# Performance work log

Hardware: AMD Instinct MI355X
Metric: run time of the kernel (lower is better)

The kernel has to match this reference:

```python
import jax, jax.numpy as jnp
import numpy as np

B, C, H, W = 16, 256, 32, 32
EPS = 1e-6


def setup_inputs() -> dict:
    key = jax.random.key(0)
    ks = jax.random.split(key, 6)
    s = 1.0 / np.sqrt(C)  # conv-like init scale
    return {
        "x": jax.random.normal(ks[0], (B, C, H, W), dtype=jnp.float32),
        "ln_w": jnp.ones((C,), dtype=jnp.float32),
        "ln_b": jnp.zeros((C,), dtype=jnp.float32),
        "wq": jax.random.normal(ks[1], (C, C), dtype=jnp.float32) * s,
        "bq": jnp.zeros((C,), dtype=jnp.float32),
        "wk": jax.random.normal(ks[2], (C, C), dtype=jnp.float32) * s,
        "bk": jnp.zeros((C,), dtype=jnp.float32),
        "wv": jax.random.normal(ks[3], (C, C), dtype=jnp.float32) * s,
        "bv": jnp.zeros((C,), dtype=jnp.float32),
        "wp": jax.random.normal(ks[4], (C, C), dtype=jnp.float32) * s,
        "bp": jnp.zeros((C,), dtype=jnp.float32),
    }


def reference(x, ln_w, ln_b, wq, bq, wk, bk, wv, bv, wp, bp):
    b, c, h, w = x.shape
    n = h * w
    # LayerNorm2d: normalize over channel dim (biased variance)
    mean = jnp.mean(x, axis=1, keepdims=True)
    var = jnp.var(x, axis=1, keepdims=True)
    hn = (x - mean) / jnp.sqrt(var + EPS)
    hn = hn * ln_w[None, :, None, None] + ln_b[None, :, None, None]
    hn = hn.reshape(b, c, n)  # [B, C, N]
    # 1x1 convs == channel matmuls; tokens layout [B, N, C]
    q = jnp.einsum('oc,bcn->bno', wq, hn) + bq  # [B, N, C]
    k = jnp.einsum('oc,bcn->bon', wk, hn) + bk[None, :, None]  # [B, C, N]
    v = jnp.einsum('oc,bcn->bno', wv, hn) + bv  # [B, N, C]
    scale = c ** (-0.5)
    attn = jnp.einsum('bnc,bcm->bnm', q, k) * scale  # [B, N, N]
    attn = jax.nn.softmax(attn, axis=-1)
    # dropout is identity in eval mode (deterministic reference)
    out = jnp.einsum('bnm,bmc->bnc', attn, v)  # [B, N, C]
    out = jnp.einsum('oc,bnc->bon', wp, out) + bp[None, :, None]  # [B, C, N]
    out = out.reshape(b, c, h, w)
    return x + out
```

## Files before the change

kernel.cpp:

```cpp
#include <hip/hip_runtime.h>
#include <hip/hip_bf16.h>
#include <stdint.h>

typedef __attribute__((ext_vector_type(8))) short bf8_t;
typedef __attribute__((ext_vector_type(4))) short s4_t;
typedef __attribute__((ext_vector_type(4))) float f4_t;
typedef __attribute__((ext_vector_type(16))) float f16x_t;
typedef unsigned short u16;

#define GLOAD16(g, l) __builtin_amdgcn_global_load_lds(                                  \
    (const __attribute__((address_space(1))) void*)(g),                                  \
    (__attribute__((address_space(3))) void*)(l), 16, 0, 0)

__device__ __forceinline__ u16 f2bf(float f) {
    union { float f; unsigned u; } c; c.f = f;
    unsigned u = c.u;
    return (u16)((u + 0x7fffu + ((u >> 16) & 1u)) >> 16);
}

__device__ __forceinline__ unsigned cvt_pk_bf16(float lo, float hi_) {
    unsigned r;
    asm("v_cvt_pk_bf16_f32 %0, %1, %2" : "=v"(r) : "v"(lo), "v"(hi_));
    return r;
}

__global__ void prep_kernel(const float* __restrict__ wq, const float* __restrict__ wk,
                            const float* __restrict__ wv, const float* __restrict__ wp,
                            const float* __restrict__ bq, const float* __restrict__ bk,
                            const float* __restrict__ bv,
                            u16* __restrict__ wcat, u16* __restrict__ wpb,
                            float* __restrict__ biasc) {
    int idx = blockIdx.x * 256 + threadIdx.x;
    if (idx < 196608) {
        int o = idx >> 8, c = idx & 255;
        float v = (o < 256) ? wq[o * 256 + c]
                : (o < 512) ? wk[(o - 256) * 256 + c]
                            : wv[(o - 512) * 256 + c];
        wcat[idx] = f2bf(v);
    } else if (idx < 262144) {
        wpb[idx - 196608] = f2bf(wp[idx - 196608]);
    } else if (idx < 262912) {
        int i = idx - 262144;
        biasc[i] = (i < 256) ? bq[i] : (i < 512) ? bk[i - 256] : bv[i - 512];
    }
}

__global__ __launch_bounds__(512) void ln_kernel(const float* __restrict__ x,
                                                 const float* __restrict__ lw,
                                                 const float* __restrict__ lb,
                                                 u16* __restrict__ hn) {
    int tid = threadIdx.x;
    int tl = tid & 63, cg = tid >> 6;
    int tok = blockIdx.x * 64 + tl;
    int b = tok >> 10, n = tok & 1023;
    const float* xb = x + (size_t)b * 262144 + n;
    int ch0 = cg * 32;
    float v[32];
    float s = 0.f, s2 = 0.f;
    #pragma unroll
    for (int j = 0; j < 32; j++) {
        v[j] = xb[(size_t)(ch0 + j) * 1024];
        s += v[j]; s2 += v[j] * v[j];
    }
    __shared__ float2 red[8][64];
    red[cg][tl] = make_float2(s, s2);
    __syncthreads();
    s = 0.f; s2 = 0.f;
    #pragma unroll
    for (int g = 0; g < 8; g++) { float2 p = red[g][tl]; s += p.x; s2 += p.y; }
    float mean = s * 0.00390625f;
    float var  = s2 * 0.00390625f - mean * mean;
    float rstd = rsqrtf(var + 1e-6f);
    u16* hr = hn + (size_t)tok * 256 + ch0;
    #pragma unroll
    for (int j8 = 0; j8 < 4; j8++) {
        bf8_t pk;
        #pragma unroll
        for (int j = 0; j < 8; j++) {
            int c = j8 * 8 + j;
            float y = (v[c] - mean) * rstd * lw[ch0 + c] + lb[ch0 + c];
            pk[j] = (short)f2bf(y);
        }
        *(bf8_t*)&hr[j8 * 8] = pk;
    }
}

template <int EPI>
__global__ __launch_bounds__(256, 2) void gemm_bt(
    const u16* __restrict__ A, const u16* __restrict__ B, void* __restrict__ Cp,
    int lda, int ldb, int ldc, int nk,
    long sA, long sB, long sC,
    const float* __restrict__ aux1, const float* __restrict__ aux2,
    u16* __restrict__ ktp, u16* __restrict__ vtp) {
    __shared__ u16 lsA[128 * 32];
    __shared__ u16 lsB[128 * 32];
    const int tid = threadIdx.x;
    const int z = blockIdx.z;
    const int m0 = blockIdx.x * 128, n0 = blockIdx.y * 128;
    const int lane = tid & 63;
    const int w = tid >> 6, wm = w >> 1, wn = w & 1;
    const int lm = lane & 15, lg = lane >> 4;
    const int sr = tid >> 2, sc = (tid & 3) * 8;

    const u16* ga = A + (size_t)z * sA + (size_t)(m0 + sr) * lda + sc;
    const u16* gb = B + (size_t)z * sB + (size_t)(n0 + sr) * ldb + sc;
    u16* la  = &lsA[sr * 32 + sc];
    u16* lb2 = &lsB[sr * 32 + sc];

    f4_t acc[4][4];
    #pragma unroll
    for (int i = 0; i < 4; i++)
        #pragma unroll
        for (int j = 0; j < 4; j++) acc[i][j] = (f4_t)0.0f;

    for (int kt = 0; kt < nk; ++kt) {
        GLOAD16(ga, la);
        GLOAD16(ga + (size_t)64 * lda, la + 64 * 32);
        GLOAD16(gb, lb2);
        GLOAD16(gb + (size_t)64 * ldb, lb2 + 64 * 32);
        ga += 32; gb += 32;
        __syncthreads();
        bf8_t af[4], bfv[4];
        #pragma unroll
        for (int i = 0; i < 4; i++)
            af[i] = *(const bf8_t*)&lsA[(wm * 64 + i * 16 + lm) * 32 + lg * 8];
        #pragma unroll
        for (int i = 0; i < 4; i++)
            bfv[i] = *(const bf8_t*)&lsB[(wn * 64 + i * 16 + lm) * 32 + lg * 8];
        #pragma unroll
        for (int i = 0; i < 4; i++)
            #pragma unroll
            for (int j = 0; j < 4; j++)
                acc[i][j] = __builtin_amdgcn_mfma_f32_16x16x32_bf16(af[i], bfv[j], acc[i][j], 0, 0, 0);
        __syncthreads();
    }

    const int rb = m0 + wm * 64 + lg * 4;
    const int cb = n0 + wn * 64 + lm;
    #pragma unroll
    for (int i = 0; i < 4; i++)
        #pragma unroll
        for (int j = 0; j < 4; j++)
            #pragma unroll
            for (int r = 0; r < 4; r++) {
                int row = rb + i * 16 + r;
                int col = cb + j * 16;
                float v = acc[i][j][r];
                if (EPI == 0) {
                    float val = v + aux1[col];
                    int bb = row >> 10, n = row & 1023;
                    if (col < 256) {
                        ((u16*)Cp)[(size_t)row * 256 + col] = f2bf(val * 0.0625f);
                    } else if (col < 512) {
                        int c = col - 256;
                        ktp[(((size_t)bb * 32 + (c >> 3)) * 1024 + n) * 8 + (c & 7)] = f2bf(val);
                    } else {
                        int d = col - 512;
                        vtp[(((size_t)bb * 128 + (n >> 3)) * 256 + d) * 8 + (n & 7)] = f2bf(val);
                    }
                } else {
                    size_t idx = (size_t)z * sC + (size_t)row * ldc + col;
                    ((float*)Cp)[idx] = v + aux1[row] + aux2[idx];
                }
            }
}

__global__ __launch_bounds__(512)
__attribute__((amdgpu_waves_per_eu(2, 2)))
void flash_kernel(const u16* __restrict__ qbuf,
                  const u16* __restrict__ kt,
                  const u16* __restrict__ vt3,
                  u16* __restrict__ O) {
    __shared__ u16 K_lds[2][2][32 * 32 * 8];
    __shared__ u16 V_lds[2][2][4 * 256 * 8];
    __shared__ float mstat[2][32], lstat[2][32];

    const int flat = blockIdx.x;
    const int xcd = flat & 7, idx = flat >> 3;
    const int b = (xcd << 1) | (idx & 1);
    const int qb = idx >> 1;
    const int tid = threadIdx.x;
    const int wv = tid >> 6, lane = tid & 63;
    const int hi = lane >> 5, lq = lane & 31;
    const int qw = wv & 1, dw = (wv >> 1) & 1, g = wv >> 2;

    const int qrow = qb * 64 + qw * 32 + lq;
    const u16* qptr = qbuf + (size_t)(b * 1024 + qrow) * 256 + hi * 8;
    bf8_t qf[16];
    #pragma unroll
    for (int tc = 0; tc < 16; tc++) qf[tc] = *(const bf8_t*)(qptr + tc * 16);

    float m_r = -1e30f, l_r = 0.f;
    f16x_t o_acc[4];
    #pragma unroll
    for (int dt = 0; dt < 4; dt++) o_acc[dt] = (f16x_t)0.0f;

#define STAGE(T, BUF)                                                                     \
    {                                                                                     \
        _Pragma("unroll")                                                                 \
        for (int g2 = 0; g2 < 2; g2++) {                                                  \
            _Pragma("unroll")                                                             \
            for (int it = 0; it < 2; it++) {                                              \
                int cid = it * 512 + tid;                                                 \
                int chunk = cid >> 5, kvl = cid & 31;                                     \
                const u16* gk = kt + (((size_t)b * 32 + chunk) * 1024                     \
                                      + g2 * 512 + (T) * 32 + kvl) * 8;                   \
                GLOAD16(gk, &K_lds[g2][BUF][cid * 8]);                                    \
            }                                                                             \
            _Pragma("unroll")                                                             \
            for (int it = 0; it < 2; it++) {                                              \
                int cid = it * 512 + tid;                                                 \
                int kc = cid >> 8, d = cid & 255;                                         \
                const u16* gv = vt3 + (((size_t)b * 128 + g2 * 64 + (T) * 4 + kc) * 256   \
                                       + d) * 8;                                          \
                GLOAD16(gv, &V_lds[g2][BUF][cid * 8]);                                    \
            }                                                                             \
        }                                                                                 \
    }

    STAGE(0, 0);
    STAGE(1, 1);
    asm volatile("s_waitcnt vmcnt(8)" ::: "memory");
    __builtin_amdgcn_s_barrier();

    for (int t = 0; t < 16; ++t) {
        const int buf = t & 1;

        const u16* kb = &K_lds[g][buf][0];
        bf8_t kf[16];
        #pragma unroll
        for (int tc = 0; tc < 16; tc++)
            kf[tc] = *(const bf8_t*)(kb + ((tc * 2 + hi) * 32 + lq) * 8);

        f16x_t s0 = (f16x_t)0.0f, s1 = (f16x_t)0.0f;
        __builtin_amdgcn_s_setprio(1);
        #pragma unroll
        for (int tc = 0; tc < 8; tc++) {
            s0 = __builtin_amdgcn_mfma_f32_32x32x16_bf16(kf[2 * tc],     qf[2 * tc],     s0, 0, 0, 0);
            s1 = __builtin_amdgcn_mfma_f32_32x32x16_bf16(kf[2 * tc + 1], qf[2 * tc + 1], s1, 0, 0, 0);
        }
        __builtin_amdgcn_s_setprio(0);

        const u16* vb = &V_lds[g][buf][0];
        bf8_t vf[8];
        #pragma unroll
        for (int dt = 0; dt < 4; dt++) {
            int vrow = dw * 128 + dt * 32 + lq;
            vf[2 * dt]     = *(const bf8_t*)(vb + (hi * 256 + vrow) * 8);
            vf[2 * dt + 1] = *(const bf8_t*)(vb + ((2 + hi) * 256 + vrow) * 8);
        }

        f16x_t s = s0 + s1;

        float m01 = fmaxf(s[0], s[1]),   m23 = fmaxf(s[2], s[3]);
        float m45 = fmaxf(s[4], s[5]),   m67 = fmaxf(s[6], s[7]);
        float m89 = fmaxf(s[8], s[9]),   mab = fmaxf(s[10], s[11]);
        float mcd = fmaxf(s[12], s[13]), mef = fmaxf(s[14], s[15]);
        float pm = fmaxf(fmaxf(fmaxf(m01, m23), fmaxf(m45, m67)),
                         fmaxf(fmaxf(m89, mab), fmaxf(mcd, mef)));
        float tm = fmaxf(pm, __shfl_xor(pm, 32));
        if (__ballot(tm > m_r + 8.0f)) {
            float mn = fmaxf(m_r, tm);
            float corr = __expf(m_r - mn);
            m_r = mn; l_r *= corr;
            #pragma unroll
            for (int dt = 0; dt < 4; dt++)
                #pragma unroll
                for (int r = 0; r < 16; r++) o_acc[dt][r] *= corr;
        }
        float sum = 0.f;
        #pragma unroll
        for (int r = 0; r < 16; r++) { s[r] = __expf(s[r] - m_r); sum += s[r]; }
        l_r += sum;

        unsigned pw[8];
        #pragma unroll
        for (int j = 0; j < 8; j++) pw[j] = cvt_pk_bf16(s[2 * j], s[2 * j + 1]);
        unsigned px[8];
        #pragma unroll
        for (int j = 0; j < 8; j++) px[j] = __shfl_xor((int)pw[j], 32);
        union { unsigned w[4]; bf8_t v; } f0, f1;
        if (hi == 0) {
            f0.w[0] = pw[0]; f0.w[1] = pw[1]; f0.w[2] = px[0]; f0.w[3] = px[1];
            f1.w[0] = pw[4]; f1.w[1] = pw[5]; f1.w[2] = px[4]; f1.w[3] = px[5];
        } else {
            f0.w[0] = px[2]; f0.w[1] = px[3]; f0.w[2] = pw[2]; f0.w[3] = pw[3];
            f1.w[0] = px[6]; f1.w[1] = px[7]; f1.w[2] = pw[6]; f1.w[3] = pw[7];
        }

        asm volatile("s_waitcnt lgkmcnt(0)" ::: "memory");
        __builtin_amdgcn_s_barrier();
        if (t < 14) STAGE(t + 2, buf);

        __builtin_amdgcn_s_setprio(1);
        #pragma unroll
        for (int dt = 0; dt < 4; dt++) {
            o_acc[dt] = __builtin_amdgcn_mfma_f32_32x32x16_bf16(vf[2 * dt],     f0.v, o_acc[dt], 0, 0, 0);
            o_acc[dt] = __builtin_amdgcn_mfma_f32_32x32x16_bf16(vf[2 * dt + 1], f1.v, o_acc[dt], 0, 0, 0);
        }
        __builtin_amdgcn_s_setprio(0);

        if (t < 15) {
            if (t < 14) { asm volatile("s_waitcnt vmcnt(8)" ::: "memory"); }
            else        { asm volatile("s_waitcnt vmcnt(0)" ::: "memory"); }
            __builtin_amdgcn_s_barrier();
        }
    }

    __syncthreads();

    float l_tot = l_r + __shfl_xor(l_r, 32);
    float* obuf = (float*)&K_lds[0][0][0];
    float* rb = obuf + (qw * 2 + dw) * 4096;
    if (g == 1) {
        #pragma unroll
        for (int dt = 0; dt < 4; dt++)
            #pragma unroll
            for (int r = 0; r < 16; r++) {
                int drow = dt * 32 + (r & 3) + 8 * (r >> 2) + 4 * hi;
                rb[drow * 32 + lq] = o_acc[dt][r];
            }
        if (dw == 0 && hi == 0) { mstat[qw][lq] = m_r; lstat[qw][lq] = l_tot; }
    }
    __syncthreads();
    if (g == 0) {
        float m1 = mstat[qw][lq], l1 = lstat[qw][lq];
        float mm = fmaxf(m_r, m1);
        float a0 = __expf(m_r - mm), a1 = __expf(m1 - mm);
        float inv = 1.0f / (a0 * l_tot + a1 * l1);
        u16* bounce = (u16*)&V_lds[0][0][0] + (qw * 2 + dw) * (32 * 136);
        #pragma unroll
        for (int dt = 0; dt < 4; dt++)
            #pragma unroll
            for (int r = 0; r < 16; r++) {
                int drow = dt * 32 + (r & 3) + 8 * (r >> 2) + 4 * hi;
                float val = (a0 * o_acc[dt][r] + a1 * rb[drow * 32 + lq]) * inv;
                bounce[lq * 136 + drow] = f2bf(val);
            }
        asm volatile("s_waitcnt lgkmcnt(0)" ::: "memory");
        #pragma unroll
        for (int it = 0; it < 4; it++) {
            int qloc = it * 8 + (lane >> 3);
            int dch = (lane & 7) * 16;
            bf8_t lo8 = *(const bf8_t*)&bounce[qloc * 136 + dch];
            bf8_t hi8 = *(const bf8_t*)&bounce[qloc * 136 + dch + 8];
            u16* dst = O + (size_t)(b * 1024 + qb * 64 + qw * 32 + qloc) * 256 + dw * 128 + dch;
            *(bf8_t*)dst = lo8;
            *(bf8_t*)(dst + 8) = hi8;
        }
    }
#undef STAGE
}

extern "C" void kernel_launch(void* const* d_in, const int* in_sizes, int n_in,
                              void* d_out, int out_size, void* d_ws, size_t ws_size,
                              hipStream_t stream) {
    (void)in_sizes; (void)n_in; (void)out_size; (void)ws_size;
    const float* x   = (const float*)d_in[0];
    const float* lnw = (const float*)d_in[1];
    const float* lnb = (const float*)d_in[2];
    const float* wq  = (const float*)d_in[3];
    const float* bq  = (const float*)d_in[4];
    const float* wk  = (const float*)d_in[5];
    const float* bk  = (const float*)d_in[6];
    const float* wv  = (const float*)d_in[7];
    const float* bv  = (const float*)d_in[8];
    const float* wp  = (const float*)d_in[9];
    const float* bp  = (const float*)d_in[10];
    float* out = (float*)d_out;

    char* ws = (char*)d_ws;
    u16*   wcat  = (u16*)(ws);
    u16*   wpb   = (u16*)(ws + 0x60000);
    float* biasc = (float*)(ws + 0x80000);
    u16*   hn    = (u16*)(ws + 0x90000);
    u16*   qbuf  = (u16*)(ws + 0x890000);
    u16*   kt    = (u16*)(ws + 0x1090000);
    u16*   vt3   = (u16*)(ws + 0x1890000);
    u16*   O     = (u16*)(ws + 0x2090000);

    prep_kernel<<<1028, 256, 0, stream>>>(wq, wk, wv, wp, bq, bk, bv, wcat, wpb, biasc);
    ln_kernel<<<256, 512, 0, stream>>>(x, lnw, lnb, hn);
    gemm_bt<0><<<dim3(128, 6, 1), 256, 0, stream>>>(hn, wcat, qbuf, 256, 256, 768, 8,
                                                    0, 0, 0, biasc, nullptr, kt, vt3);
    flash_kernel<<<256, 512, 0, stream>>>(qbuf, kt, vt3, O);
    gemm_bt<3><<<dim3(2, 8, 16), 256, 0, stream>>>(wpb, O, out, 256, 256, 1024, 8,
                                                   0, 262144, 262144, bp, x,
                                                   nullptr, nullptr);
}
```

Before: 82.98 us.

## Fuse output projection and residual add into flash attention epilogue

```diff
diff --git a/kernel.cpp b/kernel.cpp
--- a/kernel.cpp
+++ b/kernel.cpp
@@ -28,7 +28,7 @@
                             const float* __restrict__ wv, const float* __restrict__ wp,
                             const float* __restrict__ bq, const float* __restrict__ bk,
                             const float* __restrict__ bv,
-                            u16* __restrict__ wcat, u16* __restrict__ wpb,
+                            u16* __restrict__ wcat, u16* __restrict__ wpt,
                             float* __restrict__ biasc) {
     int idx = blockIdx.x * 256 + threadIdx.x;
     if (idx < 196608) {
@@ -38,7 +38,9 @@
                             : wv[(o - 512) * 256 + c];
         wcat[idx] = f2bf(v);
     } else if (idx < 262144) {
-        wpb[idx - 196608] = f2bf(wp[idx - 196608]);
+        int i = idx - 196608;
+        int o = i >> 8, d = i & 255;
+        wpt[(((d >> 3) * 256) + o) * 8 + (d & 7)] = f2bf(wp[i]);
     } else if (idx < 262912) {
         int i = idx - 262144;
         biasc[i] = (i < 256) ? bq[i] : (i < 512) ? bk[i - 256] : bv[i - 512];
@@ -85,25 +87,21 @@
     }
 }
 
-template <int EPI>
-__global__ __launch_bounds__(256, 2) void gemm_bt(
-    const u16* __restrict__ A, const u16* __restrict__ B, void* __restrict__ Cp,
-    int lda, int ldb, int ldc, int nk,
-    long sA, long sB, long sC,
-    const float* __restrict__ aux1, const float* __restrict__ aux2,
+__global__ __launch_bounds__(256, 2) void gemm_qkv(
+    const u16* __restrict__ A, const u16* __restrict__ B, u16* __restrict__ Cp,
+    const float* __restrict__ aux1,
     u16* __restrict__ ktp, u16* __restrict__ vtp) {
     __shared__ u16 lsA[128 * 32];
     __shared__ u16 lsB[128 * 32];
     const int tid = threadIdx.x;
-    const int z = blockIdx.z;
     const int m0 = blockIdx.x * 128, n0 = blockIdx.y * 128;
     const int lane = tid & 63;
     const int w = tid >> 6, wm = w >> 1, wn = w & 1;
     const int lm = lane & 15, lg = lane >> 4;
     const int sr = tid >> 2, sc = (tid & 3) * 8;
 
-    const u16* ga = A + (size_t)z * sA + (size_t)(m0 + sr) * lda + sc;
-    const u16* gb = B + (size_t)z * sB + (size_t)(n0 + sr) * ldb + sc;
+    const u16* ga = A + (size_t)(m0 + sr) * 256 + sc;
+    const u16* gb = B + (size_t)(n0 + sr) * 256 + sc;
     u16* la  = &lsA[sr * 32 + sc];
     u16* lb2 = &lsB[sr * 32 + sc];
 
@@ -113,11 +111,11 @@
         #pragma unroll
         for (int j = 0; j < 4; j++) acc[i][j] = (f4_t)0.0f;
 
-    for (int kt = 0; kt < nk; ++kt) {
+    for (int kt = 0; kt < 8; ++kt) {
         GLOAD16(ga, la);
-        GLOAD16(ga + (size_t)64 * lda, la + 64 * 32);
+        GLOAD16(ga + (size_t)64 * 256, la + 64 * 32);
         GLOAD16(gb, lb2);
-        GLOAD16(gb + (size_t)64 * ldb, lb2 + 64 * 32);
+        GLOAD16(gb + (size_t)64 * 256, lb2 + 64 * 32);
         ga += 32; gb += 32;
         __syncthreads();
         bf8_t af[4], bfv[4];
@@ -145,22 +143,16 @@
             for (int r = 0; r < 4; r++) {
                 int row = rb + i * 16 + r;
                 int col = cb + j * 16;
-                float v = acc[i][j][r];
-                if (EPI == 0) {
-                    float val = v + aux1[col];
-                    int bb = row >> 10, n = row & 1023;
-                    if (col < 256) {
-                        ((u16*)Cp)[(size_t)row * 256 + col] = f2bf(val * 0.0625f);
-                    } else if (col < 512) {
-                        int c = col - 256;
-                        ktp[(((size_t)bb * 32 + (c >> 3)) * 1024 + n) * 8 + (c & 7)] = f2bf(val);
-                    } else {
-                        int d = col - 512;
-                        vtp[(((size_t)bb * 128 + (n >> 3)) * 256 + d) * 8 + (n & 7)] = f2bf(val);
-                    }
+                float val = acc[i][j][r] + aux1[col];
+                int bb = row >> 10, n = row & 1023;
+                if (col < 256) {
+                    Cp[(size_t)row * 256 + col] = f2bf(val * 0.0625f);
+                } else if (col < 512) {
+                    int c = col - 256;
+                    ktp[(((size_t)bb * 32 + (c >> 3)) * 1024 + n) * 8 + (c & 7)] = f2bf(val);
                 } else {
-                    size_t idx = (size_t)z * sC + (size_t)row * ldc + col;
-                    ((float*)Cp)[idx] = v + aux1[row] + aux2[idx];
+                    int d = col - 512;
+                    vtp[(((size_t)bb * 128 + (n >> 3)) * 256 + d) * 8 + (n & 7)] = f2bf(val);
                 }
             }
 }
@@ -170,7 +162,10 @@
 void flash_kernel(const u16* __restrict__ qbuf,
                   const u16* __restrict__ kt,
                   const u16* __restrict__ vt3,
-                  u16* __restrict__ O) {
+                  const u16* __restrict__ wpt,
+                  const float* __restrict__ bp,
+                  const float* __restrict__ x,
+                  float* __restrict__ out) {
     __shared__ u16 K_lds[2][2][32 * 32 * 8];
     __shared__ u16 V_lds[2][2][4 * 256 * 8];
     __shared__ float mstat[2][32], lstat[2][32];
@@ -323,31 +318,47 @@
         if (dw == 0 && hi == 0) { mstat[qw][lq] = m_r; lstat[qw][lq] = l_tot; }
     }
     __syncthreads();
+
+    bf8_t wpf[16];
+    #pragma unroll
+    for (int tc = 0; tc < 16; tc++)
+        wpf[tc] = *(const bf8_t*)(wpt + (((tc * 2 + hi) * 256) + wv * 32 + lq) * 8);
+
+    u16* O16 = (u16*)&V_lds[0][0][0];
     if (g == 0) {
         float m1 = mstat[qw][lq], l1 = lstat[qw][lq];
         float mm = fmaxf(m_r, m1);
         float a0 = __expf(m_r - mm), a1 = __expf(m1 - mm);
         float inv = 1.0f / (a0 * l_tot + a1 * l1);
-        u16* bounce = (u16*)&V_lds[0][0][0] + (qw * 2 + dw) * (32 * 136);
         #pragma unroll
         for (int dt = 0; dt < 4; dt++)
             #pragma unroll
             for (int r = 0; r < 16; r++) {
                 int drow = dt * 32 + (r & 3) + 8 * (r >> 2) + 4 * hi;
+                int d = dw * 128 + drow;
                 float val = (a0 * o_acc[dt][r] + a1 * rb[drow * 32 + lq]) * inv;
-                bounce[lq * 136 + drow] = f2bf(val);
+                O16[((d >> 3) * 64 + qw * 32 + lq) * 8 + (d & 7)] = f2bf(val);
             }
-        asm volatile("s_waitcnt lgkmcnt(0)" ::: "memory");
-        #pragma unroll
-        for (int it = 0; it < 4; it++) {
-            int qloc = it * 8 + (lane >> 3);
-            int dch = (lane & 7) * 16;
-            bf8_t lo8 = *(const bf8_t*)&bounce[qloc * 136 + dch];
-            bf8_t hi8 = *(const bf8_t*)&bounce[qloc * 136 + dch + 8];
-            u16* dst = O + (size_t)(b * 1024 + qb * 64 + qw * 32 + qloc) * 256 + dw * 128 + dch;
-            *(bf8_t*)dst = lo8;
-            *(bf8_t*)(dst + 8) = hi8;
-        }
+    }
+    __syncthreads();
+
+    f16x_t p0 = (f16x_t)0.0f, p1 = (f16x_t)0.0f;
+    __builtin_amdgcn_s_setprio(1);
+    #pragma unroll
+    for (int tc = 0; tc < 16; tc++) {
+        bf8_t of0 = *(const bf8_t*)(O16 + ((tc * 2 + hi) * 64 + lq) * 8);
+        bf8_t of1 = *(const bf8_t*)(O16 + ((tc * 2 + hi) * 64 + 32 + lq) * 8);
+        p0 = __builtin_amdgcn_mfma_f32_32x32x16_bf16(wpf[tc], of0, p0, 0, 0, 0);
+        p1 = __builtin_amdgcn_mfma_f32_32x32x16_bf16(wpf[tc], of1, p1, 0, 0, 0);
+    }
+    __builtin_amdgcn_s_setprio(0);
+    #pragma unroll
+    for (int r = 0; r < 16; r++) {
+        int crow = wv * 32 + (r & 3) + 8 * (r >> 2) + 4 * hi;
+        size_t base = ((size_t)b * 256 + crow) * 1024 + qb * 64;
+        float bpv = bp[crow];
+        out[base + lq]      = p0[r] + bpv + x[base + lq];
+        out[base + 32 + lq] = p1[r] + bpv + x[base + 32 + lq];
     }
 #undef STAGE
 }
@@ -371,20 +382,15 @@
 
     char* ws = (char*)d_ws;
     u16*   wcat  = (u16*)(ws);
-    u16*   wpb   = (u16*)(ws + 0x60000);
+    u16*   wpt   = (u16*)(ws + 0x60000);
     float* biasc = (float*)(ws + 0x80000);
     u16*   hn    = (u16*)(ws + 0x90000);
     u16*   qbuf  = (u16*)(ws + 0x890000);
     u16*   kt    = (u16*)(ws + 0x1090000);
     u16*   vt3   = (u16*)(ws + 0x1890000);
-    u16*   O     = (u16*)(ws + 0x2090000);
-
-    prep_kernel<<<1028, 256, 0, stream>>>(wq, wk, wv, wp, bq, bk, bv, wcat, wpb, biasc);
+
+    prep_kernel<<<1028, 256, 0, stream>>>(wq, wk, wv, wp, bq, bk, bv, wcat, wpt, biasc);
     ln_kernel<<<256, 512, 0, stream>>>(x, lnw, lnb, hn);
-    gemm_bt<0><<<dim3(128, 6, 1), 256, 0, stream>>>(hn, wcat, qbuf, 256, 256, 768, 8,
-                                                    0, 0, 0, biasc, nullptr, kt, vt3);
-    flash_kernel<<<256, 512, 0, stream>>>(qbuf, kt, vt3, O);
-    gemm_bt<3><<<dim3(2, 8, 16), 256, 0, stream>>>(wpb, O, out, 256, 256, 1024, 8,
-                                                   0, 262144, 262144, bp, x,
-                                                   nullptr, nullptr);
-}
+    gemm_qkv<<<dim3(128, 6, 1), 256, 0, stream>>>(hn, wcat, qbuf, biasc, kt, vt3);
+    flash_kernel<<<256, 512, 0, stream>>>(qbuf, kt, vt3, wpt, bp, x, out);
+}
```

Measured after the change: 75.91 us. 8.5% less time.
